# Optimization experiments

Hardware: AMD Instinct MI355X
Metric: run time of the kernel (lower is better)

The kernel has to match this reference:

```python
import jax, jax.numpy as jnp
import numpy as np

N_NODES = 100000
N_EDGES = 3200000


def _spmm(rows, cols, vals, x):
    # out[i] = sum_{e: rows[e]==i} vals[e] * x[cols[e]]
    msgs = vals[:, None] * x[cols]  # [E, F]
    return jax.ops.segment_sum(msgs, rows, num_segments=N_NODES)


def setup_inputs() -> dict:
    key = jax.random.key(0)
    ks = jax.random.split(key, 8)
    x = jax.random.normal(ks[0], (N_NODES, 256), dtype=jnp.float32)
    adj_rows = jax.random.randint(ks[1], (N_EDGES,), 0, N_NODES, dtype=jnp.int32)
    adj_cols = jax.random.randint(ks[2], (N_EDGES,), 0, N_NODES, dtype=jnp.int32)
    adj_vals = jax.random.uniform(ks[3], (N_EDGES,), dtype=jnp.float32)
    W1 = jax.random.normal(ks[4], (256, 128), dtype=jnp.float32) * (1.0 / np.sqrt(256))
    b1 = jnp.zeros((128,), dtype=jnp.float32)
    W2 = jax.random.normal(ks[5], (128, 64), dtype=jnp.float32) * (1.0 / np.sqrt(128))
    b2 = jnp.zeros((64,), dtype=jnp.float32)
    return {"x": x, "adj_rows": adj_rows, "adj_cols": adj_cols, "adj_vals": adj_vals,
            "W1": W1, "b1": b1, "W2": W2, "b2": b2}


def reference(x, adj_rows, adj_cols, adj_vals, W1, b1, W2, b2):
    # Layer 0: spmm -> linear -> relu (dropout inactive in eval)
    h = _spmm(adj_rows, adj_cols, adj_vals, x)
    h = jax.nn.relu(h @ W1 + b1)
    # Layer 1 (last layer): spmm -> linear, no activation
    h = _spmm(adj_rows, adj_cols, adj_vals, h)
    out = h @ W2 + b2
    return out  # squeeze(1) is a no-op for [N, nclass]
```

## Files before the change

kernel.cpp:

```cpp
#include <hip/hip_runtime.h>
#include <hip/hip_fp16.h>


#define RPB 480
#define NB_MAX 1024
#define PCHUNK 8192
#define EPT 32

typedef _Float16 half8 __attribute__((ext_vector_type(8)));
typedef _Float16 h2t __attribute__((ext_vector_type(2)));
typedef float floatx4 __attribute__((ext_vector_type(4)));

__global__ __launch_bounds__(256) void zero_i32_kernel(int* __restrict__ p, int n) {
    int i = blockIdx.x * 256 + threadIdx.x;
    if (i < n) p[i] = 0;
}

__global__ __launch_bounds__(256) void prep_weights_kernel(const float* __restrict__ W1,
                                                           const float* __restrict__ W2,
                                                           __half* __restrict__ W1T,
                                                           h2t* __restrict__ pk) {
    int i = blockIdx.x * 256 + threadIdx.x;
    if (i < 256 * 128) {
        int k = i >> 7, n = i & 127;
        W1T[n * 256 + k] = __float2half_rn(W1[i]);
    } else {
        int j = i - 256 * 128;
        if (j < 4096) {
            int kk = j >> 6, c = j & 63;
            h2t v;
            v[0] = (_Float16)W2[(2 * kk) * 64 + c];
            v[1] = (_Float16)W2[(2 * kk + 1) * 64 + c];
            pk[j] = v;
        }
    }
}

__global__ __launch_bounds__(256) void transpose_w_kernel(const float* __restrict__ W,
                                                          __half* __restrict__ WT,
                                                          int K, int N) {
    int i = blockIdx.x * 256 + threadIdx.x;
    if (i < K * N) {
        int k = i / N, n = i % N;
        WT[n * K + k] = __float2half_rn(W[i]);
    }
}

__global__ __launch_bounds__(256) void bucket_hist_kernel(const int* __restrict__ rows,
                                                          int* __restrict__ gcnt,
                                                          int nE, int nB) {
    __shared__ int hist[NB_MAX];
    const int t = threadIdx.x;
    const int c0 = blockIdx.x * PCHUNK;
    const int c1 = min(c0 + PCHUNK, nE);
    for (int b = t; b < nB; b += 256) hist[b] = 0;
    __syncthreads();
    for (int e = c0 + t; e < c1; e += 256) atomicAdd(&hist[rows[e] / RPB], 1);
    __syncthreads();
    for (int b = t; b < nB; b += 256) {
        int c = hist[b];
        if (c) atomicAdd(&gcnt[b], c);
    }
}

__global__ __launch_bounds__(1024) void bucket_scan_kernel(const int* __restrict__ gcnt,
                                                           int* __restrict__ boff,
                                                           int* __restrict__ gcur,
                                                           int* __restrict__ off,
                                                           int nB, int nN) {
    __shared__ int part[1024];
    int t = threadIdx.x;
    int v = (t < nB) ? gcnt[t] : 0;
    part[t] = v;
    __syncthreads();
    for (int d = 1; d < 1024; d <<= 1) {
        int add = (t >= d) ? part[t - d] : 0;
        __syncthreads();
        part[t] += add;
        __syncthreads();
    }
    if (t < nB) {
        int excl = part[t] - v;
        boff[t] = excl;
        gcur[t] = excl;
    }
    if (t == 1023) {
        boff[nB] = part[1023];
        off[nN] = part[1023];
    }
}

__global__ __launch_bounds__(256) void partition_kernel(const int* __restrict__ rows,
                                                        const int* __restrict__ cols,
                                                        const float* __restrict__ vals,
                                                        int* __restrict__ gcur,
                                                        int2* __restrict__ eb1,
                                                        int nE, int nB) {
    __shared__ int hist[NB_MAX];
    __shared__ int cur[NB_MAX];
    const int t = threadIdx.x;
    const int c0 = blockIdx.x * PCHUNK;
    for (int b = t; b < nB; b += 256) hist[b] = 0;
    __syncthreads();
    int myr[EPT];
#pragma unroll
    for (int j = 0; j < EPT; ++j) {
        int e = c0 + t + 256 * j;
        int r = (e < nE) ? rows[e] : -1;
        myr[j] = r;
        if (r >= 0) atomicAdd(&hist[r / RPB], 1);
    }
    __syncthreads();
    for (int b = t; b < nB; b += 256) {
        int c = hist[b];
        cur[b] = c ? atomicAdd(&gcur[b], c) : 0;
    }
    __syncthreads();
#pragma unroll
    for (int j = 0; j < EPT; ++j) {
        int r = myr[j];
        if (r >= 0) {
            int e = c0 + t + 256 * j;
            int bk = r / RPB;
            int rl = r - bk * RPB;
            int pos = atomicAdd(&cur[bk], 1);
            eb1[pos] = make_int2((cols[e] & 0x1FFFF) | (rl << 17), __float_as_int(vals[e]));
        }
    }
}

__global__ __launch_bounds__(512) void fine_scatter_kernel(const int* __restrict__ boff,
                                                           const int2* __restrict__ eb1,
                                                           int2* __restrict__ eb2,
                                                           int* __restrict__ off,
                                                           int nN) {
    __shared__ int hist[RPB];
    __shared__ int sc[RPB];
    __shared__ int cur[RPB];
    const int b = blockIdx.x;
    const int row0 = b * RPB;
    const int nr = min(RPB, nN - row0);
    const int t = threadIdx.x;
    const int s = boff[b];
    const int e = boff[b + 1];

    if (t < RPB) hist[t] = 0;
    __syncthreads();
    for (int i = s + t; i < e; i += 512)
        atomicAdd(&hist[((unsigned)eb1[i].x) >> 17], 1);
    __syncthreads();

    int myc = (t < RPB) ? hist[t] : 0;
    if (t < RPB) sc[t] = myc;
    __syncthreads();
    for (int d = 1; d < RPB; d <<= 1) {
        int add = (t < RPB && t >= d) ? sc[t - d] : 0;
        __syncthreads();
        if (t < RPB) sc[t] += add;
        __syncthreads();
    }
    if (t < RPB) {
        int excl = s + sc[t] - myc;
        cur[t] = excl;
        if (t < nr) off[row0 + t] = excl;
    }
    __syncthreads();

    for (int i = s + t; i < e; i += 512) {
        int2 ed = eb1[i];
        unsigned x = (unsigned)ed.x;
        int pos = atomicAdd(&cur[x >> 17], 1);
        eb2[pos] = make_int2((int)(x & 0x1FFFF), ed.y);
    }
}

__global__ __launch_bounds__(256) void spmm_fused_kernel(const int* __restrict__ off,
                                                         const int2* __restrict__ eb,
                                                         const __half* __restrict__ Y,
                                                         const float* __restrict__ b1,
                                                         const h2t* __restrict__ pk,
                                                         __half* __restrict__ Y2, int nN) {
    __shared__ h2t w2s[64 * 64];
    __shared__ h2t hs[4][64];
    const int t = threadIdx.x;
#pragma unroll
    for (int i = 0; i < 16; ++i) w2s[i * 256 + t] = pk[i * 256 + t];
    __syncthreads();

    const int row = blockIdx.x * 4 + (t >> 6);
    const int wv = t >> 6;
    const int lane = t & 63;

    if (row < nN) {
        float2 acc = make_float2(b1[lane * 2], b1[lane * 2 + 1]);
        int s = off[row];
        int e1 = off[row + 1];
        for (int base = s; base < e1; base += 64) {
            int n = min(64, e1 - base);
            int2 my = (lane < n) ? eb[base + lane] : make_int2(0, 0);
            int j = 0;
            for (; j + 4 <= n; j += 4) {
                int c0 = __shfl(my.x, j + 0), c1 = __shfl(my.x, j + 1);
                int c2 = __shfl(my.x, j + 2), c3 = __shfl(my.x, j + 3);
                float v0 = __int_as_float(__shfl(my.y, j + 0));
                float v1 = __int_as_float(__shfl(my.y, j + 1));
                float v2 = __int_as_float(__shfl(my.y, j + 2));
                float v3 = __int_as_float(__shfl(my.y, j + 3));
                float2 y0 = __half22float2(*((const __half2*)(Y + (size_t)c0 * 128) + lane));
                float2 y1 = __half22float2(*((const __half2*)(Y + (size_t)c1 * 128) + lane));
                float2 y2 = __half22float2(*((const __half2*)(Y + (size_t)c2 * 128) + lane));
                float2 y3 = __half22float2(*((const __half2*)(Y + (size_t)c3 * 128) + lane));
                acc.x = fmaf(v0, y0.x, acc.x); acc.y = fmaf(v0, y0.y, acc.y);
                acc.x = fmaf(v1, y1.x, acc.x); acc.y = fmaf(v1, y1.y, acc.y);
                acc.x = fmaf(v2, y2.x, acc.x); acc.y = fmaf(v2, y2.y, acc.y);
                acc.x = fmaf(v3, y3.x, acc.x); acc.y = fmaf(v3, y3.y, acc.y);
            }
            for (; j < n; ++j) {
                int c = __shfl(my.x, j);
                float v = __int_as_float(__shfl(my.y, j));
                float2 y = __half22float2(*((const __half2*)(Y + (size_t)c * 128) + lane));
                acc.x = fmaf(v, y.x, acc.x);
                acc.y = fmaf(v, y.y, acc.y);
            }
        }
        h2t hv;
        hv[0] = (_Float16)fmaxf(acc.x, 0.f);
        hv[1] = (_Float16)fmaxf(acc.y, 0.f);
        hs[wv][lane] = hv;

        float o = 0.f;
#pragma unroll 8
        for (int kk = 0; kk < 64; ++kk) {
            h2t a = hs[wv][kk];
            h2t b = w2s[kk * 64 + lane];
#if __has_builtin(__builtin_amdgcn_fdot2)
            o = __builtin_amdgcn_fdot2(a, b, o, false);
#else
            o = fmaf((float)a[0], (float)b[0], o);
            o = fmaf((float)a[1], (float)b[1], o);
#endif
        }
        Y2[(size_t)row * 64 + lane] = __float2half_rn(o);
    }
}

__global__ __launch_bounds__(256) void spmm_csr64_kernel(const int* __restrict__ off,
                                                         const int2* __restrict__ eb,
                                                         const __half* __restrict__ Y,
                                                         const float* __restrict__ bias,
                                                         float* __restrict__ out, int nN) {
    int row = blockIdx.x * 4 + (threadIdx.x >> 6);
    if (row >= nN) return;
    int lane = threadIdx.x & 63;
    int s = off[row];
    int e1 = off[row + 1];

    float acc = bias[lane];
    for (int base = s; base < e1; base += 64) {
        int n = min(64, e1 - base);
        int2 my = (lane < n) ? eb[base + lane] : make_int2(0, 0);
        int j = 0;
        for (; j + 4 <= n; j += 4) {
            int c0 = __shfl(my.x, j + 0), c1 = __shfl(my.x, j + 1);
            int c2 = __shfl(my.x, j + 2), c3 = __shfl(my.x, j + 3);
            float v0 = __int_as_float(__shfl(my.y, j + 0));
            float v1 = __int_as_float(__shfl(my.y, j + 1));
            float v2 = __int_as_float(__shfl(my.y, j + 2));
            float v3 = __int_as_float(__shfl(my.y, j + 3));
            float y0 = __half2float(Y[(size_t)c0 * 64 + lane]);
            float y1 = __half2float(Y[(size_t)c1 * 64 + lane]);
            float y2 = __half2float(Y[(size_t)c2 * 64 + lane]);
            float y3 = __half2float(Y[(size_t)c3 * 64 + lane]);
            acc = fmaf(v0, y0, acc);
            acc = fmaf(v1, y1, acc);
            acc = fmaf(v2, y2, acc);
            acc = fmaf(v3, y3, acc);
        }
        for (; j < n; ++j) {
            int c = __shfl(my.x, j);
            float v = __int_as_float(__shfl(my.y, j));
            acc = fmaf(v, __half2float(Y[(size_t)c * 64 + lane]), acc);
        }
    }
    out[(size_t)row * 64 + lane] = acc;
}

__global__ __launch_bounds__(256) void init_bias_kernel(float* __restrict__ out,
                                                        const float* __restrict__ bias,
                                                        int fmask, size_t total) {
    size_t i = (size_t)blockIdx.x * 256 + threadIdx.x;
    if (i < total) out[i] = bias[i & fmask];
}

template <int F>
__global__ __launch_bounds__(256) void spmm_atomic_kernel(const int* __restrict__ rows,
                                                          const int* __restrict__ cols,
                                                          const float* __restrict__ vals,
                                                          const __half* __restrict__ Y,
                                                          float* __restrict__ out, int nE) {
    int e = blockIdx.x * 4 + (threadIdx.x >> 6);
    if (e >= nE) return;
    int lane = threadIdx.x & 63;
    int r = rows[e];
    int c = cols[e];
    float v = vals[e];
    if (F == 128) {
        float2 y = __half22float2(*((const __half2*)(Y + (size_t)c * 128) + lane));
        float* op = out + (size_t)r * 128 + lane * 2;
        unsafeAtomicAdd(op, v * y.x);
        unsafeAtomicAdd(op + 1, v * y.y);
    } else {
        float y = __half2float(Y[(size_t)c * F + lane]);
        unsafeAtomicAdd(out + (size_t)r * F + lane, v * y);
    }
}

template <int NN, int KK, bool RELU_IN>
__global__ __launch_bounds__(256) void gemm_mfma_kernel(const float* __restrict__ A,
                                                        const __half* __restrict__ BT,
                                                        __half* __restrict__ C, int nrows) {
    constexpr int MT = 64, KT = 64, KP = KT + 8;
    __shared__ __half As[MT * KP];
    __shared__ __half Bs[NN * KP];
    const int tid = threadIdx.x;
    const int wid = tid >> 6, lane = tid & 63;
    const int row0 = blockIdx.x * MT;
    const int wr = wid & 1, wc = wid >> 1;
    constexpr int WCT = NN / 32;
    const int lrow = lane & 15, q = lane >> 4;

    floatx4 acc[2][WCT];
#pragma unroll
    for (int rt = 0; rt < 2; ++rt)
#pragma unroll
        for (int ct = 0; ct < WCT; ++ct)
#pragma unroll
            for (int i = 0; i < 4; ++i) acc[rt][ct][i] = 0.f;

    for (int kt = 0; kt < KK; kt += KT) {
#pragma unroll
        for (int it = 0; it < MT * KT / 4 / 256; ++it) {
            int i4 = it * 256 + tid;
            int m = i4 >> 4;
            int kk = (i4 & 15) << 2;
            int gr = row0 + m;
            float4 v = make_float4(0.f, 0.f, 0.f, 0.f);
            if (gr < nrows) v = *(const float4*)(A + (size_t)gr * KK + kt + kk);
            if (RELU_IN) {
                v.x = fmaxf(v.x, 0.f); v.y = fmaxf(v.y, 0.f);
                v.z = fmaxf(v.z, 0.f); v.w = fmaxf(v.w, 0.f);
            }
            __half h0 = __float2half_rn(v.x), h1 = __float2half_rn(v.y);
            __half h2 = __float2half_rn(v.z), h3 = __float2half_rn(v.w);
            ushort4 u = make_ushort4(*(unsigned short*)&h0, *(unsigned short*)&h1,
                                     *(unsigned short*)&h2, *(unsigned short*)&h3);
            *(ushort4*)(As + m * KP + kk) = u;
        }
#pragma unroll
        for (int it = 0; it < NN * KT / 4 / 256; ++it) {
            int i4 = it * 256 + tid;
            int n = i4 >> 4;
            int kk = (i4 & 15) << 2;
            *(ushort4*)(Bs + n * KP + kk) =
                *(const ushort4*)(BT + (size_t)n * KK + kt + kk);
        }
        __syncthreads();

#pragma unroll
        for (int ks = 0; ks < KT; ks += 32) {
            half8 a0 = *(half8*)(As + (wr * 32 + lrow) * KP + ks + q * 8);
            half8 a1 = *(half8*)(As + (wr * 32 + 16 + lrow) * KP + ks + q * 8);
#pragma unroll
            for (int ct = 0; ct < WCT; ++ct) {
                half8 b = *(half8*)(Bs + (wc * (NN / 2) + ct * 16 + lrow) * KP + ks + q * 8);
                acc[0][ct] = __builtin_amdgcn_mfma_f32_16x16x32_f16(a0, b, acc[0][ct], 0, 0, 0);
                acc[1][ct] = __builtin_amdgcn_mfma_f32_16x16x32_f16(a1, b, acc[1][ct], 0, 0, 0);
            }
        }
        __syncthreads();
    }

#pragma unroll
    for (int rt = 0; rt < 2; ++rt)
#pragma unroll
        for (int ct = 0; ct < WCT; ++ct)
#pragma unroll
            for (int r = 0; r < 4; ++r) {
                int gr = row0 + wr * 32 + rt * 16 + q * 4 + r;
                if (gr < nrows)
                    C[(size_t)gr * NN + wc * (NN / 2) + ct * 16 + lrow] =
                        __float2half_rn(acc[rt][ct][r]);
            }
}

extern "C" void kernel_launch(void* const* d_in, const int* in_sizes, int n_in,
                              void* d_out, int out_size, void* d_ws, size_t ws_size,
                              hipStream_t stream) {
    const float* x    = (const float*)d_in[0];
    const int*   rows = (const int*)d_in[1];
    const int*   cols = (const int*)d_in[2];
    const float* vals = (const float*)d_in[3];
    const float* W1   = (const float*)d_in[4];
    const float* b1   = (const float*)d_in[5];
    const float* W2   = (const float*)d_in[6];
    const float* b2   = (const float*)d_in[7];
    float* out = (float*)d_out;

    const int nN = in_sizes[0] / 256;
    const int nE = in_sizes[1];
    const int nB = (nN + RPB - 1) / RPB;

    char* w = (char*)d_ws;
    __half* Y1h = (__half*)w;   w += (size_t)nN * 128 * 2;
    float*  H1  = (float*)w;    w += (size_t)nN * 128 * 4;
    __half* Y2h = (__half*)H1;
    __half* W1T = (__half*)w;   w += (size_t)256 * 128 * 2;
    __half* W2T = (__half*)w;   w += (size_t)128 * 64 * 2;
    h2t*    pk  = (h2t*)w;      w += (size_t)4096 * 4;
    int*  off   = (int*)w;      w += ((size_t)nN + 4) * 4;
    int*  gcnt  = (int*)w;      w += (size_t)NB_MAX * 4;
    int*  boff  = (int*)w;      w += (size_t)(NB_MAX + 4) * 4;
    int*  gcur  = (int*)w;      w += (size_t)NB_MAX * 4;
    int2* eb1   = (int2*)w;     w += (size_t)nE * 8;
    int2* eb2   = (int2*)w;     w += (size_t)nE * 8;
    size_t need = (size_t)(w - (char*)d_ws);

    const int mblocks  = (nN + 63) / 64;
    const int pblocks  = (nE + PCHUNK - 1) / PCHUNK;
    const int rblocks  = (nN + 3) / 4;
    const int eblocks4 = (nE + 3) / 4;

    if (ws_size >= need && nN <= (1 << 17) && nB <= NB_MAX) {
        prep_weights_kernel<<<(256 * 128 + 4096 + 255) / 256, 256, 0, stream>>>(W1, W2, W1T, pk);
        gemm_mfma_kernel<128, 256, false><<<mblocks, 256, 0, stream>>>(x, W1T, Y1h, nN);

        zero_i32_kernel<<<(nB + 255) / 256, 256, 0, stream>>>(gcnt, nB);
        bucket_hist_kernel<<<pblocks, 256, 0, stream>>>(rows, gcnt, nE, nB);
        bucket_scan_kernel<<<1, 1024, 0, stream>>>(gcnt, boff, gcur, off, nB, nN);
        partition_kernel<<<pblocks, 256, 0, stream>>>(rows, cols, vals, gcur, eb1, nE, nB);
        fine_scatter_kernel<<<nB, 512, 0, stream>>>(boff, eb1, eb2, off, nN);

        spmm_fused_kernel<<<rblocks, 256, 0, stream>>>(off, eb2, Y1h, b1, pk, Y2h, nN);
        spmm_csr64_kernel<<<rblocks, 256, 0, stream>>>(off, eb2, Y2h, b2, out, nN);
    } else {
        transpose_w_kernel<<<(256 * 128 + 255) / 256, 256, 0, stream>>>(W1, W1T, 256, 128);
        transpose_w_kernel<<<(128 * 64 + 255) / 256, 256, 0, stream>>>(W2, W2T, 128, 64);
        gemm_mfma_kernel<128, 256, false><<<mblocks, 256, 0, stream>>>(x, W1T, Y1h, nN);
        size_t totH1 = (size_t)nN * 128;
        init_bias_kernel<<<(int)((totH1 + 255) / 256), 256, 0, stream>>>(H1, b1, 127, totH1);
        spmm_atomic_kernel<128><<<eblocks4, 256, 0, stream>>>(rows, cols, vals, Y1h, H1, nE);
        gemm_mfma_kernel<64, 128, true><<<mblocks, 256, 0, stream>>>(H1, W2T, Y1h, nN);
        size_t totOut = (size_t)nN * 64;
        init_bias_kernel<<<(int)((totOut + 255) / 256), 256, 0, stream>>>(out, b2, 63, totOut);
        spmm_atomic_kernel<64><<<eblocks4, 256, 0, stream>>>(rows, cols, vals, Y1h, out, nE);
    }
}
```

Measured before the change: 520.3 us.

## Vectorize SpMM gathers to 16-byte loads with lane-group edge splitting

Both CSR SpMM kernels now have each lane load 8 fp16 features (16 bytes) per gathered row and split the wavefront into groups that handle different edges at once. Per-group partial sums are combined with xor shuffles before bias, ReLU and the store. This aims to cut memory instructions and raise bytes in flight per gather, at the cost of more registers and shuffle reductions. The zero-init kernel is also folded into the weight-prep kernel, and fine_scatter moves to 1024-thread blocks.

After: 478.9 us. 1.09x faster.

```diff
diff --git a/kernel.cpp b/kernel.cpp
--- a/kernel.cpp
+++ b/kernel.cpp
@@ -11,28 +11,25 @@
 typedef _Float16 h2t __attribute__((ext_vector_type(2)));
 typedef float floatx4 __attribute__((ext_vector_type(4)));
 
-__global__ __launch_bounds__(256) void zero_i32_kernel(int* __restrict__ p, int n) {
-    int i = blockIdx.x * 256 + threadIdx.x;
-    if (i < n) p[i] = 0;
-}
-
 __global__ __launch_bounds__(256) void prep_weights_kernel(const float* __restrict__ W1,
                                                            const float* __restrict__ W2,
                                                            __half* __restrict__ W1T,
-                                                           h2t* __restrict__ pk) {
+                                                           h2t* __restrict__ pk,
+                                                           int* __restrict__ gcnt) {
     int i = blockIdx.x * 256 + threadIdx.x;
     if (i < 256 * 128) {
         int k = i >> 7, n = i & 127;
         W1T[n * 256 + k] = __float2half_rn(W1[i]);
+    } else if (i < 256 * 128 + 4096) {
+        int j = i - 256 * 128;
+        int kk = j >> 6, c = j & 63;
+        h2t v;
+        v[0] = (_Float16)W2[(2 * kk) * 64 + c];
+        v[1] = (_Float16)W2[(2 * kk + 1) * 64 + c];
+        pk[j] = v;
     } else {
-        int j = i - 256 * 128;
-        if (j < 4096) {
-            int kk = j >> 6, c = j & 63;
-            h2t v;
-            v[0] = (_Float16)W2[(2 * kk) * 64 + c];
-            v[1] = (_Float16)W2[(2 * kk + 1) * 64 + c];
-            pk[j] = v;
-        }
+        int j = i - (256 * 128 + 4096);
+        if (j < NB_MAX) gcnt[j] = 0;
     }
 }
 
@@ -129,11 +126,11 @@
     }
 }
 
-__global__ __launch_bounds__(512) void fine_scatter_kernel(const int* __restrict__ boff,
-                                                           const int2* __restrict__ eb1,
-                                                           int2* __restrict__ eb2,
-                                                           int* __restrict__ off,
-                                                           int nN) {
+__global__ __launch_bounds__(1024) void fine_scatter_kernel(const int* __restrict__ boff,
+                                                            const int2* __restrict__ eb1,
+                                                            int2* __restrict__ eb2,
+                                                            int* __restrict__ off,
+                                                            int nN) {
     __shared__ int hist[RPB];
     __shared__ int sc[RPB];
     __shared__ int cur[RPB];
@@ -146,7 +143,7 @@
 
     if (t < RPB) hist[t] = 0;
     __syncthreads();
-    for (int i = s + t; i < e; i += 512)
+    for (int i = s + t; i < e; i += 1024)
         atomicAdd(&hist[((unsigned)eb1[i].x) >> 17], 1);
     __syncthreads();
 
@@ -166,7 +163,7 @@
     }
     __syncthreads();
 
-    for (int i = s + t; i < e; i += 512) {
+    for (int i = s + t; i < e; i += 1024) {
         int2 ed = eb1[i];
         unsigned x = (unsigned)ed.x;
         int pos = atomicAdd(&cur[x >> 17], 1);
@@ -192,41 +189,58 @@
     const int lane = t & 63;
 
     if (row < nN) {
-        float2 acc = make_float2(b1[lane * 2], b1[lane * 2 + 1]);
+        const int fg = lane & 15;
+        const int g = lane >> 4;
+        float acc[8];
+#pragma unroll
+        for (int p = 0; p < 8; ++p) acc[p] = 0.f;
+
         int s = off[row];
         int e1 = off[row + 1];
         for (int base = s; base < e1; base += 64) {
             int n = min(64, e1 - base);
             int2 my = (lane < n) ? eb[base + lane] : make_int2(0, 0);
-            int j = 0;
-            for (; j + 4 <= n; j += 4) {
-                int c0 = __shfl(my.x, j + 0), c1 = __shfl(my.x, j + 1);
-                int c2 = __shfl(my.x, j + 2), c3 = __shfl(my.x, j + 3);
-                float v0 = __int_as_float(__shfl(my.y, j + 0));
-                float v1 = __int_as_float(__shfl(my.y, j + 1));
-                float v2 = __int_as_float(__shfl(my.y, j + 2));
-                float v3 = __int_as_float(__shfl(my.y, j + 3));
-                float2 y0 = __half22float2(*((const __half2*)(Y + (size_t)c0 * 128) + lane));
-                float2 y1 = __half22float2(*((const __half2*)(Y + (size_t)c1 * 128) + lane));
-                float2 y2 = __half22float2(*((const __half2*)(Y + (size_t)c2 * 128) + lane));
-                float2 y3 = __half22float2(*((const __half2*)(Y + (size_t)c3 * 128) + lane));
-                acc.x = fmaf(v0, y0.x, acc.x); acc.y = fmaf(v0, y0.y, acc.y);
-                acc.x = fmaf(v1, y1.x, acc.x); acc.y = fmaf(v1, y1.y, acc.y);
-                acc.x = fmaf(v2, y2.x, acc.x); acc.y = fmaf(v2, y2.y, acc.y);
-                acc.x = fmaf(v3, y3.x, acc.x); acc.y = fmaf(v3, y3.y, acc.y);
+            for (int j = 0; j < n; j += 8) {
+                int i0 = j + g;
+                int i1 = j + 4 + g;
+                int s0 = (i0 < n) ? i0 : j;
+                int s1 = (i1 < n) ? i1 : j;
+                int c0 = __shfl(my.x, s0);
+                int c1 = __shfl(my.x, s1);
+                float v0 = __int_as_float(__shfl(my.y, s0));
+                float v1 = __int_as_float(__shfl(my.y, s1));
+                if (i0 >= n) v0 = 0.f;
+                if (i1 >= n) v1 = 0.f;
+                half8 y0 = *(const half8*)(Y + ((size_t)c0 << 7) + (fg << 3));
+                half8 y1 = *(const half8*)(Y + ((size_t)c1 << 7) + (fg << 3));
+#pragma unroll
+                for (int p = 0; p < 8; ++p) acc[p] = fmaf(v0, (float)y0[p], acc[p]);
+#pragma unroll
+                for (int p = 0; p < 8; ++p) acc[p] = fmaf(v1, (float)y1[p], acc[p]);
             }
-            for (; j < n; ++j) {
-                int c = __shfl(my.x, j);
-                float v = __int_as_float(__shfl(my.y, j));
-                float2 y = __half22float2(*((const __half2*)(Y + (size_t)c * 128) + lane));
-                acc.x = fmaf(v, y.x, acc.x);
-                acc.y = fmaf(v, y.y, acc.y);
+        }
+#pragma unroll
+        for (int p = 0; p < 8; ++p) acc[p] += __shfl_xor(acc[p], 16);
+#pragma unroll
+        for (int p = 0; p < 8; ++p) acc[p] += __shfl_xor(acc[p], 32);
+
+        if (g == 0) {
+            floatx4 ba = *(const floatx4*)(b1 + fg * 8);
+            floatx4 bb = *(const floatx4*)(b1 + fg * 8 + 4);
+            float f[8];
+#pragma unroll
+            for (int p = 0; p < 4; ++p) f[p] = fmaxf(acc[p] + ba[p], 0.f);
+#pragma unroll
+            for (int p = 0; p < 4; ++p) f[4 + p] = fmaxf(acc[4 + p] + bb[p], 0.f);
+#pragma unroll
+            for (int p = 0; p < 4; ++p) {
+                h2t pr;
+                pr[0] = (_Float16)f[2 * p];
+                pr[1] = (_Float16)f[2 * p + 1];
+                hs[wv][fg * 4 + p] = pr;
             }
         }
-        h2t hv;
-        hv[0] = (_Float16)fmaxf(acc.x, 0.f);
-        hv[1] = (_Float16)fmaxf(acc.y, 0.f);
-        hs[wv][lane] = hv;
+        __builtin_amdgcn_sched_barrier(0);
 
         float o = 0.f;
 #pragma unroll 8
@@ -252,37 +266,56 @@
     int row = blockIdx.x * 4 + (threadIdx.x >> 6);
     if (row >= nN) return;
     int lane = threadIdx.x & 63;
+    const int fg = lane & 7;
+    const int g = lane >> 3;
+
+    float acc[8];
+#pragma unroll
+    for (int p = 0; p < 8; ++p) acc[p] = 0.f;
+
     int s = off[row];
     int e1 = off[row + 1];
-
-    float acc = bias[lane];
     for (int base = s; base < e1; base += 64) {
         int n = min(64, e1 - base);
         int2 my = (lane < n) ? eb[base + lane] : make_int2(0, 0);
-        int j = 0;
-        for (; j + 4 <= n; j += 4) {
-            int c0 = __shfl(my.x, j + 0), c1 = __shfl(my.x, j + 1);
-            int c2 = __shfl(my.x, j + 2), c3 = __shfl(my.x, j + 3);
-            float v0 = __int_as_float(__shfl(my.y, j + 0));
-            float v1 = __int_as_float(__shfl(my.y, j + 1));
-            float v2 = __int_as_float(__shfl(my.y, j + 2));
-            float v3 = __int_as_float(__shfl(my.y, j + 3));
-            float y0 = __half2float(Y[(size_t)c0 * 64 + lane]);
-            float y1 = __half2float(Y[(size_t)c1 * 64 + lane]);
-            float y2 = __half2float(Y[(size_t)c2 * 64 + lane]);
-            float y3 = __half2float(Y[(size_t)c3 * 64 + lane]);
-            acc = fmaf(v0, y0, acc);
-            acc = fmaf(v1, y1, acc);
-            acc = fmaf(v2, y2, acc);
-            acc = fmaf(v3, y3, acc);
-        }
-        for (; j < n; ++j) {
-            int c = __shfl(my.x, j);
-            float v = __int_as_float(__shfl(my.y, j));
-            acc = fmaf(v, __half2float(Y[(size_t)c * 64 + lane]), acc);
-        }
-    }
-    out[(size_t)row * 64 + lane] = acc;
+        for (int j = 0; j < n; j += 16) {
+            int i0 = j + g;
+            int i1 = j + 8 + g;
+            int s0 = (i0 < n) ? i0 : j;
+            int s1 = (i1 < n) ? i1 : j;
+            int c0 = __shfl(my.x, s0);
+            int c1 = __shfl(my.x, s1);
+            float v0 = __int_as_float(__shfl(my.y, s0));
+            float v1 = __int_as_float(__shfl(my.y, s1));
+            if (i0 >= n) v0 = 0.f;
+            if (i1 >= n) v1 = 0.f;
+            half8 y0 = *(const half8*)(Y + ((size_t)c0 << 6) + (fg << 3));
+            half8 y1 = *(const half8*)(Y + ((size_t)c1 << 6) + (fg << 3));
+#pragma unroll
+            for (int p = 0; p < 8; ++p) acc[p] = fmaf(v0, (float)y0[p], acc[p]);
+#pragma unroll
+            for (int p = 0; p < 8; ++p) acc[p] = fmaf(v1, (float)y1[p], acc[p]);
+        }
+    }
+#pragma unroll
+    for (int p = 0; p < 8; ++p) acc[p] += __shfl_xor(acc[p], 8);
+#pragma unroll
+    for (int p = 0; p < 8; ++p) acc[p] += __shfl_xor(acc[p], 16);
+#pragma unroll
+    for (int p = 0; p < 8; ++p) acc[p] += __shfl_xor(acc[p], 32);
+
+    if (g == 0) {
+        floatx4 ba = *(const floatx4*)(bias + fg * 8);
+        floatx4 bb = *(const floatx4*)(bias + fg * 8 + 4);
+        floatx4 o0, o1;
+#pragma unroll
+        for (int p = 0; p < 4; ++p) o0[p] = acc[p] + ba[p];
+#pragma unroll
+        for (int p = 0; p < 4; ++p) o1[p] = acc[4 + p] + bb[p];
+        float* op = out + (size_t)row * 64 + fg * 8;
+        *(floatx4*)op = o0;
+        *(floatx4*)(op + 4) = o1;
+    }
 }
 
 __global__ __launch_bounds__(256) void init_bias_kernel(float* __restrict__ out,
@@ -431,14 +464,14 @@
     const int eblocks4 = (nE + 3) / 4;
 
     if (ws_size >= need && nN <= (1 << 17) && nB <= NB_MAX) {
-        prep_weights_kernel<<<(256 * 128 + 4096 + 255) / 256, 256, 0, stream>>>(W1, W2, W1T, pk);
+        prep_weights_kernel<<<(256 * 128 + 4096 + NB_MAX + 255) / 256, 256, 0, stream>>>(
+            W1, W2, W1T, pk, gcnt);
         gemm_mfma_kernel<128, 256, false><<<mblocks, 256, 0, stream>>>(x, W1T, Y1h, nN);
 
-        zero_i32_kernel<<<(nB + 255) / 256, 256, 0, stream>>>(gcnt, nB);
         bucket_hist_kernel<<<pblocks, 256, 0, stream>>>(rows, gcnt, nE, nB);
         bucket_scan_kernel<<<1, 1024, 0, stream>>>(gcnt, boff, gcur, off, nB, nN);
         partition_kernel<<<pblocks, 256, 0, stream>>>(rows, cols, vals, gcur, eb1, nE, nB);
-        fine_scatter_kernel<<<nB, 512, 0, stream>>>(boff, eb1, eb2, off, nN);
+        fine_scatter_kernel<<<nB, 1024, 0, stream>>>(boff, eb1, eb2, off, nN);
 
         spmm_fused_kernel<<<rblocks, 256, 0, stream>>>(off, eb2, Y1h, b1, pk, Y2h, nN);
         spmm_csr64_kernel<<<rblocks, 256, 0, stream>>>(off, eb2, Y2h, b2, out, nN);
```
